# Performance work log

Measured on AMD Instinct MI355X. Metric: run time of the kernel, lower is better.

## Reference

```python
import jax, jax.numpy as jnp
import numpy as np

PRIOR = 0.1      # prior_prob
P_NOISE = 0.05   # p
DAMPING = 0.5
BETA = 0.3
EPS = 1e-10


def compute_likelihood(Y_edges, prod_fail_others, beta_edges, p):
    p_sick_if_healthy = 1.0 - prod_fail_others
    p_sick_if_infected = 1.0 - prod_fail_others * (1.0 - beta_edges)
    normal_if_sick = (1.0 - p) * p_sick_if_healthy
    sick_if_sick = (1.0 - p) * p_sick_if_infected
    normal_if_normal = p * p_sick_if_healthy + (1.0 - p_sick_if_healthy)
    sick_if_normal = p * p_sick_if_infected + (1.0 - p_sick_if_infected)
    is_pos = Y_edges == 1
    L0 = jnp.where(is_pos, normal_if_sick, normal_if_normal)
    L1 = jnp.where(is_pos, sick_if_sick, sick_if_normal)
    return L0, L1


def setup_inputs() -> dict:
    key = jax.random.key(0)
    k1, k2, k3 = jax.random.split(key, 3)
    num_tests = 100000
    num_patients = 200000
    num_edges = 12800000
    Y_obs = jax.random.randint(k1, (num_tests,), 0, 2, dtype=jnp.int32)
    idx_i = jax.random.randint(k2, (num_edges,), 0, num_tests, dtype=jnp.int32)
    idx_j = jax.random.randint(k3, (num_edges,), 0, num_patients, dtype=jnp.int32)
    # beta_edges = 1.0 on diagonal entries, beta elsewhere (as in __init__)
    beta_edges = jnp.where(idx_i == idx_j, 1.0, BETA).astype(jnp.float32)
    return {"Y_obs": Y_obs, "idx_i": idx_i, "idx_j": idx_j,
            "beta_edges": beta_edges, "max_iters": 50,
            "num_patients": num_patients}


def reference(Y_obs, idx_i, idx_j, beta_edges, max_iters, num_patients):
    num_tests = Y_obs.shape[0]
    num_edges = idx_i.shape[0]
    Y_edges = Y_obs[idx_i]  # [E]

    def step(carry, it):
        msg_j_to_i, old0, old1, _ = carry
        # test-side aggregation: prob all other patients failed to infect test i
        fail = 1.0 - beta_edges * msg_j_to_i
        log_fail = jnp.log(fail + EPS)
        tot_log_fail = jax.ops.segment_sum(log_fail, idx_i, num_segments=num_tests)
        prod_fail_others = jnp.exp(tot_log_fail[idx_i]) / (fail + EPS)
        new0, new1 = compute_likelihood(Y_edges, prod_fail_others, beta_edges, P_NOISE)
        first = it == 0
        m0 = jnp.where(first, new0, DAMPING * new0 + (1.0 - DAMPING) * old0)
        m1 = jnp.where(first, new1, DAMPING * new1 + (1.0 - DAMPING) * old1)
        old0_n, old1_n = m0, m1  # stored BEFORE normalization, as in torch code
        norm = m0 + m1 + EPS
        log_m0 = jnp.log(m0 / norm + EPS)
        log_m1 = jnp.log(m1 / norm + EPS)
        # patient-side aggregation
        t0 = jax.ops.segment_sum(log_m0, idx_j, num_segments=num_patients)
        t1 = jax.ops.segment_sum(log_m1, idx_j, num_segments=num_patients)
        log_b0 = jnp.log(1.0 - PRIOR) + t0
        log_b1 = jnp.log(PRIOR) + t1
        beliefs = jax.nn.sigmoid(log_b1 - log_b0)  # = 1/(1+exp(lb0-lb1))
        msg_next = jax.nn.sigmoid((log_b1[idx_j] - log_m1) - (log_b0[idx_j] - log_m0))
        return (msg_next, old0_n, old1_n, beliefs), None

    init = (jnp.full((num_edges,), PRIOR, dtype=jnp.float32),
            jnp.zeros((num_edges,), jnp.float32),
            jnp.zeros((num_edges,), jnp.float32),
            jnp.full((num_patients,), PRIOR, dtype=jnp.float32))
    (_, _, _, node_beliefs), _ = jax.lax.scan(step, init, jnp.arange(max_iters))
    return node_beliefs
```

## Files before the change

kernel.cpp:

```cpp
#include <hip/hip_runtime.h>
#include <hip/hip_fp16.h>

#define EPSF   1e-10f
#define PRIORF 0.1f
#define QF     0.95f
#define BETAF  0.3f
#define BS     256
#define WPB    4
#define CAPT   4
#define LOGIT_PRIOR (-2.1972245773362196f)
#define GSH    13
#define NG_MAX 32
#define SPAN_I 256
#define NB2_MAX 1024
#define SPAN_J 128
#define NBJ_MAX 2048
#define CHA    16384
#define CHJ    8192
#define D16    0x2000u
#define JL16   0x1FFFu
#define NXCD   8
#define BSP    1024
#define WPBP   16
#define BLK_SLP 512

__device__ __forceinline__ float wave_sum(float v) {
    #pragma unroll
    for (int m = 32; m >= 1; m >>= 1) v += __shfl_xor(v, m, 64);
    return v;
}
__device__ __forceinline__ float frcp(float x) {
    return __builtin_amdgcn_rcpf(x);
}
__device__ __forceinline__ float2 unpack(__half2 h) {
    return make_float2(__low2float(h), __high2float(h));
}
__device__ __forceinline__ float calcD(float2 o) {
    float inv = frcp(o.x + o.y + EPSF);
    return __logf(o.y * inv + EPSF) - __logf(o.x * inv + EPSF);
}
__device__ __forceinline__ float sigmoidf(float x) {
    return frcp(1.0f + __expf(-x));
}

__device__ __forceinline__ int run_search(int cum, int len, int v0,
                                          int cidx, int NG, int* gout) {
    int lo = 0, hi = NG - 1;
    #pragma unroll
    for (int st = 0; st < 5; ++st) {
        int mid = (lo + hi) >> 1;
        int cmid = __shfl(cum, mid);
        int open = (lo < hi);
        int p = (cmid > cidx);
        int nhi = p ? mid : hi;
        int nlo = p ? lo : (mid + 1);
        hi = open ? nhi : hi;
        lo = open ? nlo : lo;
    }
    int cl = __shfl(cum, lo);
    int ll = __shfl(len, lo);
    int vv = __shfl(v0, lo);
    *gout = lo;
    return vv + cidx - (cl - ll);
}

__global__ __launch_bounds__(BS) void k_test(
    const int*            __restrict__ rowptrG,
    const unsigned short* __restrict__ jidx16,
    const int*            __restrict__ Y,
    const float*          __restrict__ delta,
    __half2*              __restrict__ oldm,
    int T, int NG, int first, int BPC)
{
    int lane = threadIdx.x & 63;
    int x  = blockIdx.x & (NXCD - 1);
    int mm = blockIdx.x >> 3;
    int i = (x * BPC + mm) * WPB + (threadIdx.x >> 6);
    if (i >= T) return;
    int v0 = 0, v1 = 0;
    if (lane < NG) v0 = rowptrG[(size_t)i * NG + lane];
    int l2 = lane - 32;
    if (l2 >= 0 && l2 < NG) v1 = rowptrG[(size_t)(i + 1) * NG + l2];
    int endv = __shfl(v1, 32 + lane);
    int len = (lane < NG) ? (endv - v0) : 0;
    int cum = len;
    #pragma unroll
    for (int off = 1; off < 64; off <<= 1) {
        int t = __shfl_up(cum, off);
        if (lane >= off) cum += t;
    }
    int deg = __shfl(cum, 63);
    int nch = (deg + 63) >> 6;
    int ypos = (Y[i] == 1);
    float lsum = 0.0f;

    if (deg <= 64 * CAPT) {
        int ssv[CAPT]; int ksv[CAPT]; float2 osv[CAPT]; float fsv[CAPT];
        #pragma unroll
        for (int c = 0; c < CAPT; ++c) {
            if (c >= nch) break;
            int idx = c * 64 + lane;
            int cidx = min(idx, deg - 1);
            int g;
            int s = run_search(cum, len, v0, cidx, NG, &g);
            bool act = (idx < deg);
            int k = 0; float2 o = make_float2(0.f, 0.f); float f = 1.0f;
            if (act) {
                k = jidx16[s];
                float b = (k & D16) ? 1.0f : BETAF;
                float msg;
                if (first) msg = PRIORF;
                else {
                    o = unpack(oldm[s]);
                    int j = (g << GSH) | (k & JL16);
                    msg = sigmoidf(delta[j] - calcD(o));
                }
                f = 1.0f - b * msg;
                lsum += __logf(f + EPSF);
            }
            ssv[c] = act ? s : -1; ksv[c] = k; osv[c] = o; fsv[c] = f;
        }
        float Etot = __expf(wave_sum(lsum));
        #pragma unroll
        for (int c = 0; c < CAPT; ++c) {
            if (c >= nch) break;
            int s = ssv[c];
            if (s < 0) continue;
            int k = ksv[c]; float f = fsv[c];
            float b = (k & D16) ? 1.0f : BETAF;
            float prod = Etot * frcp(f + EPSF);
            float psh = 1.0f - prod;
            float psi = 1.0f - prod * (1.0f - b);
            float L0 = ypos ? QF * psh : 1.0f - QF * psh;
            float L1 = ypos ? QF * psi : 1.0f - QF * psi;
            float m0, m1;
            if (first) { m0 = L0; m1 = L1; }
            else { float2 o = osv[c]; m0 = 0.5f * L0 + 0.5f * o.x;
                                      m1 = 0.5f * L1 + 0.5f * o.y; }
            oldm[s] = __floats2half2_rn(m0, m1);
        }
    } else {
        for (int base = 0; base < deg; base += 64) {
            int idx = base + lane;
            int cidx = min(idx, deg - 1);
            int g;
            int s = run_search(cum, len, v0, cidx, NG, &g);
            if (idx < deg) {
                int k = jidx16[s];
                float b = (k & D16) ? 1.0f : BETAF;
                float msg;
                if (first) msg = PRIORF;
                else {
                    int j = (g << GSH) | (k & JL16);
                    msg = sigmoidf(delta[j] - calcD(unpack(oldm[s])));
                }
                lsum += __logf(1.0f - b * msg + EPSF);
            }
        }
        float Etot = __expf(wave_sum(lsum));
        for (int base = 0; base < deg; base += 64) {
            int idx = base + lane;
            int cidx = min(idx, deg - 1);
            int g;
            int s = run_search(cum, len, v0, cidx, NG, &g);
            if (idx < deg) {
                int k = jidx16[s];
                float b = (k & D16) ? 1.0f : BETAF;
                float2 o = make_float2(0.f, 0.f);
                float msg;
                if (first) msg = PRIORF;
                else { o = unpack(oldm[s]);
                       int j = (g << GSH) | (k & JL16);
                       msg = sigmoidf(delta[j] - calcD(o)); }
                float f = 1.0f - b * msg;
                float prod = Etot * frcp(f + EPSF);
                float psh = 1.0f - prod;
                float psi = 1.0f - prod * (1.0f - b);
                float L0 = ypos ? QF * psh : 1.0f - QF * psh;
                float L1 = ypos ? QF * psi : 1.0f - QF * psi;
                float m0, m1;
                if (first) { m0 = L0; m1 = L1; }
                else { m0 = 0.5f * L0 + 0.5f * o.x; m1 = 0.5f * L1 + 0.5f * o.y; }
                oldm[s] = __floats2half2_rn(m0, m1);
            }
        }
    }
}

__global__ __launch_bounds__(BSP) void k_patient(
    const int*     __restrict__ colptr,
    const int*     __restrict__ eposJ,
    const __half2* __restrict__ oldm,
    float*         __restrict__ delta,
    float*         __restrict__ out, int P, int NG)
{
    int b = blockIdx.x;
    int x = b & (NXCD - 1);
    int r = b >> 3;
    int m = r >> 9;
    int w = r & (BLK_SLP - 1);
    int g = x + NXCD * m;
    if (g >= NG) return;
    int lane = threadIdx.x & 63;
    int p = (g << GSH) + w * WPBP + (threadIdx.x >> 6);
    if (p >= P) return;
    int u0 = colptr[p], u1 = colptr[p + 1];
    float S = 0.0f;
    for (int u = u0 + lane; u < u1; u += 64)
        S += calcD(unpack(oldm[eposJ[u]]));
    S = wave_sum(S);
    if (lane == 0) {
        float d = LOGIT_PRIOR + S;
        delta[p] = d;
        out[p] = sigmoidf(d);
    }
}

__global__ void k_zf2(int* frontG, int* front2, int* frontJ,
                      int NG, int nb2tot, int nbj) {
    int t = blockIdx.x * blockDim.x + threadIdx.x;
    if (t <= NG) frontG[t] = 0;
    if (t <= nb2tot) front2[t] = 0;
    if (t <= nbj) frontJ[t] = 0;
}

__global__ __launch_bounds__(BS) void k_binG(
    const int* __restrict__ idx_i, const int* __restrict__ idx_j,
    int* __restrict__ frontG, unsigned* __restrict__ stageA,
    int E, int NG, int capA)
{
    __shared__ int h[WPB][NG_MAX], rsv[WPB][NG_MAX], cu[WPB][NG_MAX];
    int tid = threadIdx.x;
    int w = tid >> 6, lane = tid & 63;
    if (lane < NG) { h[w][lane] = 0; cu[w][lane] = 0; }
    __syncthreads();
    int start = blockIdx.x * CHA, end = min(start + CHA, E);
    for (int e = start + tid; e < end; e += BS)
        atomicAdd(&h[w][idx_j[e] >> GSH], 1);
    __syncthreads();
    if (tid < NG) {
        int g = tid;
        int t0 = h[0][g], t1 = h[1][g], t2 = h[2][g], t3 = h[3][g];
        int tot = t0 + t1 + t2 + t3;
        int base = tot ? atomicAdd(&frontG[g], tot) : 0;
        rsv[0][g] = base;
        rsv[1][g] = base + t0;
        rsv[2][g] = base + t0 + t1;
        rsv[3][g] = base + t0 + t1 + t2;
    }
    __syncthreads();
    for (int e = start + tid; e < end; e += BS) {
        int i = idx_i[e], j = idx_j[e];
        int g = j >> GSH;
        int pos = rsv[w][g] + atomicAdd(&cu[w][g], 1);
        if (pos < capA)
            stageA[(size_t)g * capA + pos] =
                ((unsigned)i << 14) | ((unsigned)(i == j) << 13)
                | (unsigned)(j & ((1 << GSH) - 1));
    }
}

__global__ __launch_bounds__(BS) void k_binI2(
    const unsigned* __restrict__ stageA, const int* __restrict__ frontG,
    int* __restrict__ front2, unsigned* __restrict__ stage2,
    int NG, int NB2, int capA, int cap2, int chunks)
{
    int g = blockIdx.x / chunks, c = blockIdx.x % chunks;
    int n = min(frontG[g], capA);
    int start = c * 2 * CHA, end = min(start + 2 * CHA, n);
    if (start >= end) return;
    __shared__ int h[NB2_MAX], rsv[NB2_MAX], cu[NB2_MAX];
    int tid = threadIdx.x;
    for (int b = tid; b < NB2; b += BS) h[b] = 0;
    __syncthreads();
    const unsigned* rb = stageA + (size_t)g * capA;
    for (int r = start + tid; r < end; r += BS)
        atomicAdd(&h[(rb[r] >> 14) >> 8], 1);
    __syncthreads();
    for (int b = tid; b < NB2; b += BS) {
        int cc = h[b];
        rsv[b] = cc ? atomicAdd(&front2[g * NB2 + b], cc) : 0;
        cu[b] = 0;
    }
    __syncthreads();
    for (int r = start + tid; r < end; r += BS) {
        unsigned v = rb[r];
        int i = (int)(v >> 14);
        int ib = i >> 8;
        int pos = rsv[ib] + atomicAdd(&cu[ib], 1);
        if (pos < cap2)
            stage2[(size_t)(g * NB2 + ib) * cap2 + pos] =
                ((unsigned)(i & 255) << 14) | (v & 0x3FFFu);
    }
}

__global__ void k_scan_front(int* a, int n, int cap) {
    __shared__ int tmp[BS];
    __shared__ int carry;
    int tid = threadIdx.x;
    if (tid == 0) carry = 0;
    __syncthreads();
    for (int base = 0; base < n; base += BS) {
        int i = base + tid;
        int v = (i < n) ? min(a[i], cap) : 0;
        tmp[tid] = v; __syncthreads();
        for (int off = 1; off < BS; off <<= 1) {
            int x = (tid >= off) ? tmp[tid - off] : 0;
            __syncthreads();
            tmp[tid] += x;
            __syncthreads();
        }
        int c = carry;
        if (i < n) a[i] = c + tmp[tid] - v;
        __syncthreads();
        if (tid == BS - 1) carry = c + tmp[tid];
        __syncthreads();
    }
    if (tid == 0) a[n] = carry;
}

__global__ __launch_bounds__(BS) void k_csr2(
    const unsigned* __restrict__ stage2, const int* __restrict__ front2s,
    int* __restrict__ rowptrG, unsigned short* __restrict__ jidx16,
    int T, int NG, int NB2, int cap2)
{
    __shared__ int deg[SPAN_I], loff[SPAN_I], cu[SPAN_I];
    int b = blockIdx.x, tid = threadIdx.x;
    int g = b / NB2, ib = b % NB2;
    int base = front2s[b];
    int n = min(front2s[b + 1] - base, cap2);
    deg[tid] = 0;
    __syncthreads();
    const unsigned* rb = stage2 + (size_t)b * cap2;
    for (int r = tid; r < n; r += BS)
        atomicAdd(&deg[rb[r] >> 14], 1);
    __syncthreads();
    loff[tid] = deg[tid];
    __syncthreads();
    for (int off = 1; off < SPAN_I; off <<= 1) {
        int v = (tid >= off) ? loff[tid - off] : 0;
        __syncthreads();
        loff[tid] += v;
        __syncthreads();
    }
    {
        int excl = loff[tid] - deg[tid];
        int i = ib * SPAN_I + tid;
        if (i < T) rowptrG[(size_t)i * NG + g] = base + excl;
        cu[tid] = base + excl;
    }
    __syncthreads();
    for (int r = tid; r < n; r += BS) {
        unsigned v = rb[r];
        int pos = atomicAdd(&cu[v >> 14], 1);
        jidx16[pos] = (unsigned short)(v & 0x3FFFu);
    }
}

__global__ void k_fin(const int* front2s, int* rowptrG, int T, int NG, int NB2) {
    int g = threadIdx.x;
    if (g < NG) rowptrG[(size_t)T * NG + g] = front2s[(g + 1) * NB2];
}

__global__ __launch_bounds__(BS) void k_binJ(
    const unsigned short* __restrict__ jidx16,
    const int* __restrict__ front2s,
    int* __restrict__ front, unsigned int* __restrict__ stage,
    int E, int nbj, int cap, int NG, int NB2)
{
    __shared__ int h[NBJ_MAX], rsv[NBJ_MAX], cu[NBJ_MAX];
    __shared__ int ends[NG_MAX];
    int tid = threadIdx.x;
    if (tid < NG) ends[tid] = front2s[(tid + 1) * NB2];
    for (int b = tid; b < nbj; b += BS) h[b] = 0;
    __syncthreads();
    int start = blockIdx.x * CHJ, end = min(start + CHJ, E);
    for (int e = start + tid; e < end; e += BS) {
        int lo = 0, hi = NG - 1;
        while (lo < hi) { int mid = (lo + hi) >> 1;
                          if (e < ends[mid]) hi = mid; else lo = mid + 1; }
        int j = (lo << GSH) | (jidx16[e] & JL16);
        atomicAdd(&h[j >> 7], 1);
    }
    __syncthreads();
    for (int b = tid; b < nbj; b += BS) {
        int c = h[b];
        rsv[b] = c ? atomicAdd(&front[b], c) : 0;
        cu[b] = 0;
    }
    __syncthreads();
    for (int e = start + tid; e < end; e += BS) {
        int lo = 0, hi = NG - 1;
        while (lo < hi) { int mid = (lo + hi) >> 1;
                          if (e < ends[mid]) hi = mid; else lo = mid + 1; }
        int j = (lo << GSH) | (jidx16[e] & JL16);
        int bb = j >> 7;
        int pos = rsv[bb] + atomicAdd(&cu[bb], 1);
        if (pos < cap)
            stage[(size_t)bb * cap + pos] = ((unsigned)(j & 127) << 24) | (unsigned)e;
    }
}

__global__ __launch_bounds__(BS) void k_csrJ(
    const unsigned int* __restrict__ stage, const int* __restrict__ fbase,
    int* __restrict__ colptr, int* __restrict__ eposJ, int P, int E, int cap)
{
    __shared__ int deg[SPAN_J], loff[SPAN_J], cu[SPAN_J];
    int b = blockIdx.x, tid = threadIdx.x;
    int gbase = fbase[b];
    int n = min(fbase[b + 1] - gbase, cap);
    if (tid < SPAN_J) deg[tid] = 0;
    __syncthreads();
    const unsigned int* rb = stage + (size_t)b * cap;
    for (int r = tid; r < n; r += BS)
        atomicAdd(&deg[rb[r] >> 24], 1);
    __syncthreads();
    if (tid < SPAN_J) loff[tid] = deg[tid];
    __syncthreads();
    for (int off = 1; off < SPAN_J; off <<= 1) {
        int v = 0;
        if (tid < SPAN_J && tid >= off) v = loff[tid - off];
        __syncthreads();
        if (tid < SPAN_J) loff[tid] += v;
        __syncthreads();
    }
    if (tid < SPAN_J) {
        int excl = loff[tid] - deg[tid];
        int p = b * SPAN_J + tid;
        if (p < P) colptr[p] = gbase + excl;
        cu[tid] = gbase + excl;
    }
    __syncthreads();
    for (int r = tid; r < n; r += BS) {
        unsigned int v = rb[r];
        int pos = atomicAdd(&cu[v >> 24], 1);
        eposJ[pos] = (int)(v & 0xFFFFFFu);
    }
    if (b == 0 && tid == 0) colptr[P] = E;
}

extern "C" void kernel_launch(void* const* d_in, const int* in_sizes, int n_in,
                              void* d_out, int out_size, void* d_ws, size_t ws_size,
                              hipStream_t stream) {
    const int* Y     = (const int*)d_in[0];
    const int* idx_i = (const int*)d_in[1];
    const int* idx_j = (const int*)d_in[2];
    const int T = in_sizes[0];
    const int E = in_sizes[1];
    const int P = out_size;
    const int ITERS = 50;

    int* eposJ = (int*)d_in[3];

    const int NG     = (P + (1 << GSH) - 1) >> GSH;
    const int NB2    = (T + SPAN_I - 1) / SPAN_I;
    const int nb2tot = NG * NB2;
    const int nbj    = (P + SPAN_J - 1) / SPAN_J;
    long long meanA = (long long)E * (1 << GSH) / P;
    const int capA  = (int)(meanA + (meanA >> 6) + 4096);
    long long mean2 = meanA * SPAN_I / T;
    const int cap2  = (int)(mean2 + (mean2 >> 4) + 256);
    const int capJ  = E / nbj + E / (nbj * 8) + 1024;

    char* ws = (char*)d_ws;
    auto alloc = [&](size_t bytes) -> char* {
        char* p = ws; ws += (bytes + 255) & ~(size_t)255; return p;
    };
    int* rowptrG = (int*)alloc((size_t)(T + 1) * NG * 4);
    int* colptr  = (int*)alloc((size_t)(P + 1) * 4);
    int* frontG  = (int*)alloc((size_t)(NG + 1) * 4);
    int* front2  = (int*)alloc((size_t)(nb2tot + 1) * 4);
    int* frontJ  = (int*)alloc((size_t)(nbj + 1) * 4);
    size_t szA = (size_t)capA * NG * 4, szjx = (size_t)E * 2;
    char* regionA = alloc(szA > szjx ? szA : szjx);
    unsigned*       stageA = (unsigned*)regionA;
    unsigned short* jidx16 = (unsigned short*)regionA;
    size_t oldm_b = ((size_t)E * 4 + 255) & ~(size_t)255;
    size_t sz2 = (size_t)cap2 * nb2tot * 4;
    size_t szJ = (size_t)capJ * nbj * 4;
    size_t szO = oldm_b + (size_t)P * 4;
    size_t szB = sz2 > szJ ? sz2 : szJ; if (szO > szB) szB = szO;
    char* regionB = alloc(szB);
    unsigned* stage2 = (unsigned*)regionB;
    unsigned* stageJ = (unsigned*)regionB;
    __half2*  oldm   = (__half2*)regionB;
    float*    delta  = (float*)(regionB + oldm_b);
    float*    out    = (float*)d_out;

    const int zb = (nb2tot + BS) / BS + 1;
    const int chunks = (capA + 2 * CHA - 1) / (2 * CHA);
    k_zf2<<<zb, BS, 0, stream>>>(frontG, front2, frontJ, NG, nb2tot, nbj);
    k_binG<<<(E + CHA - 1) / CHA, BS, 0, stream>>>(idx_i, idx_j, frontG, stageA,
                                                   E, NG, capA);
    k_binI2<<<NG * chunks, BS, 0, stream>>>(stageA, frontG, front2, stage2,
                                            NG, NB2, capA, cap2, chunks);
    k_scan_front<<<1, BS, 0, stream>>>(front2, nb2tot, cap2);
    k_csr2<<<nb2tot, BS, 0, stream>>>(stage2, front2, rowptrG, jidx16,
                                      T, NG, NB2, cap2);
    k_fin<<<1, 64, 0, stream>>>(front2, rowptrG, T, NG, NB2);
    k_binJ<<<(E + CHJ - 1) / CHJ, BS, 0, stream>>>(jidx16, front2, frontJ, stageJ,
                                                   E, nbj, capJ, NG, NB2);
    k_scan_front<<<1, BS, 0, stream>>>(frontJ, nbj, capJ);
    k_csrJ<<<nbj, BS, 0, stream>>>(stageJ, frontJ, colptr, eposJ, P, E, capJ);

    const int BPC   = (T + WPB * NXCD - 1) / (WPB * NXCD);
    const int tgrid = NXCD * BPC;
    const int maxm  = (NG + NXCD - 1) / NXCD;
    const int pgrid = NXCD * maxm * BLK_SLP;
    for (int it = 0; it < ITERS; ++it) {
        k_test<<<tgrid, BS, 0, stream>>>(rowptrG, jidx16, Y, delta, oldm,
                                         T, NG, it == 0, BPC);
        k_patient<<<pgrid, BSP, 0, stream>>>(colptr, eposJ, oldm, delta, out,
                                             P, NG);
    }
}
```

Baseline: 9.064 ms.

## Use half-wave per patient, single shared histogram in binG, smaller chunks

The patient reduction kernel now assigns 32 lanes per patient instead of a full 64-lane wave, doubling patients per block, since average patient degree (~64) leaves lanes idle across loop iterations. The group-binning kernel drops per-wave histograms in favour of a single shared histogram per block and halves its chunk size, giving more blocks. The I-binning chunk size is decoupled into its own constant. Single-histogram atomics may add LDS contention, while the half-wave reduction cuts shuffle steps.

New measurement: 8.482 ms. 1.07x faster.

```diff
diff --git a/kernel.cpp b/kernel.cpp
--- a/kernel.cpp
+++ b/kernel.cpp
@@ -15,14 +15,15 @@
 #define NB2_MAX 1024
 #define SPAN_J 128
 #define NBJ_MAX 2048
-#define CHA    16384
+#define CHA    8192
+#define CHB    8192
 #define CHJ    8192
 #define D16    0x2000u
 #define JL16   0x1FFFu
 #define NXCD   8
 #define BSP    1024
-#define WPBP   16
-#define BLK_SLP 512
+#define WPBP   32
+#define BLK_SLP 256
 
 __device__ __forceinline__ float wave_sum(float v) {
     #pragma unroll
@@ -197,19 +198,21 @@
     int b = blockIdx.x;
     int x = b & (NXCD - 1);
     int r = b >> 3;
-    int m = r >> 9;
+    int m = r >> 8;
     int w = r & (BLK_SLP - 1);
     int g = x + NXCD * m;
     if (g >= NG) return;
     int lane = threadIdx.x & 63;
-    int p = (g << GSH) + w * WPBP + (threadIdx.x >> 6);
+    int hl = lane & 31;
+    int p = (g << GSH) + w * WPBP + ((threadIdx.x >> 6) << 1) + (lane >> 5);
     if (p >= P) return;
     int u0 = colptr[p], u1 = colptr[p + 1];
     float S = 0.0f;
-    for (int u = u0 + lane; u < u1; u += 64)
+    for (int u = u0 + hl; u < u1; u += 32)
         S += calcD(unpack(oldm[eposJ[u]]));
-    S = wave_sum(S);
-    if (lane == 0) {
+    #pragma unroll
+    for (int mm = 16; mm >= 1; mm >>= 1) S += __shfl_xor(S, mm, 64);
+    if (hl == 0) {
         float d = LOGIT_PRIOR + S;
         delta[p] = d;
         out[p] = sigmoidf(d);
@@ -229,30 +232,21 @@
     int* __restrict__ frontG, unsigned* __restrict__ stageA,
     int E, int NG, int capA)
 {
-    __shared__ int h[WPB][NG_MAX], rsv[WPB][NG_MAX], cu[WPB][NG_MAX];
+    __shared__ int h[NG_MAX], rsv[NG_MAX], cu[NG_MAX];
     int tid = threadIdx.x;
-    int w = tid >> 6, lane = tid & 63;
-    if (lane < NG) { h[w][lane] = 0; cu[w][lane] = 0; }
+    if (tid < NG) h[tid] = 0;
     __syncthreads();
     int start = blockIdx.x * CHA, end = min(start + CHA, E);
     for (int e = start + tid; e < end; e += BS)
-        atomicAdd(&h[w][idx_j[e] >> GSH], 1);
-    __syncthreads();
-    if (tid < NG) {
-        int g = tid;
-        int t0 = h[0][g], t1 = h[1][g], t2 = h[2][g], t3 = h[3][g];
-        int tot = t0 + t1 + t2 + t3;
-        int base = tot ? atomicAdd(&frontG[g], tot) : 0;
-        rsv[0][g] = base;
-        rsv[1][g] = base + t0;
-        rsv[2][g] = base + t0 + t1;
-        rsv[3][g] = base + t0 + t1 + t2;
-    }
+        atomicAdd(&h[idx_j[e] >> GSH], 1);
+    __syncthreads();
+    if (tid < NG) { int c = h[tid];
+        rsv[tid] = c ? atomicAdd(&frontG[tid], c) : 0; cu[tid] = 0; }
     __syncthreads();
     for (int e = start + tid; e < end; e += BS) {
         int i = idx_i[e], j = idx_j[e];
         int g = j >> GSH;
-        int pos = rsv[w][g] + atomicAdd(&cu[w][g], 1);
+        int pos = rsv[g] + atomicAdd(&cu[g], 1);
         if (pos < capA)
             stageA[(size_t)g * capA + pos] =
                 ((unsigned)i << 14) | ((unsigned)(i == j) << 13)
@@ -267,7 +261,7 @@
 {
     int g = blockIdx.x / chunks, c = blockIdx.x % chunks;
     int n = min(frontG[g], capA);
-    int start = c * 2 * CHA, end = min(start + 2 * CHA, n);
+    int start = c * 2 * CHB, end = min(start + 2 * CHB, n);
     if (start >= end) return;
     __shared__ int h[NB2_MAX], rsv[NB2_MAX], cu[NB2_MAX];
     int tid = threadIdx.x;
@@ -488,7 +482,7 @@
     float*    out    = (float*)d_out;
 
     const int zb = (nb2tot + BS) / BS + 1;
-    const int chunks = (capA + 2 * CHA - 1) / (2 * CHA);
+    const int chunks = (capA + 2 * CHB - 1) / (2 * CHB);
     k_zf2<<<zb, BS, 0, stream>>>(frontG, front2, frontJ, NG, nb2tot, nbj);
     k_binG<<<(E + CHA - 1) / CHA, BS, 0, stream>>>(idx_i, idx_j, frontG, stageA,
                                                    E, NG, capA);
```
